# Kernel optimization log

Measured on AMD Instinct MI355X. Metric: run time of the kernel, lower is better.

Reference implementation:

```python
import jax, jax.numpy as jnp
import numpy as np

B, S, H = 128, 512, 768      # batch, seq, encoder hidden
NL = 42                      # len(LABEL_TO_ID)
LD = 300                     # label_dim
DK, DV = 64, 768             # K_dim, V_dim
HID = 768                    # opt['hidden_dim']
P = 512                      # max_seq_length == pos_indicator
INF = 1e12                   # constant.INFINITY_NUMBER
NEG = -1e9


def gelu(x):
    return 0.5 * x * (1.0 + jax.lax.erf(x * 0.7071067811865476))


def setup_inputs() -> dict:
    key = jax.random.key(0)
    ks = jax.random.split(key, 24)
    sc = 0.02
    return {
        "inputs": jax.random.normal(ks[0], (B, S, H), jnp.float32),
        "pos_ids": jax.random.randint(ks[1], (B, S), 0, 53),
        "dep_ids": jax.random.randint(ks[2], (B, S), 0, 42),
        "subj_pos": jax.random.randint(ks[3], (B, S), 0, P + 1),
        "obj_pos": jax.random.randint(ks[4], (B, S), 0, P + 1),
        "adj": jnp.zeros((1, 1, 1), jnp.float32),  # unused by forward
        # stacked per-label Q/K projections (41 = NL-1 labels, label 0 excluded)
        "WQ": jax.random.normal(ks[5], (NL - 1, DK, H), jnp.float32) * sc,
        "bQ": jax.random.normal(ks[6], (NL - 1, DK), jnp.float32) * sc,
        "WK": jax.random.normal(ks[7], (NL - 1, DK, LD), jnp.float32) * sc,
        "bK": jax.random.normal(ks[8], (NL - 1, DK), jnp.float32) * sc,
        "WV_w": jax.random.normal(ks[9], (DV, H), jnp.float32) * sc,
        "WV_b": jax.random.normal(ks[10], (DV,), jnp.float32) * sc,
        "Wout_w": jax.random.normal(ks[11], (H, DV), jnp.float32) * sc,
        "Wout_b": jax.random.normal(ks[12], (H,), jnp.float32) * sc,
        "ln_g": jnp.ones((H,), jnp.float32),
        "ln_b": jnp.zeros((H,), jnp.float32),
        "label_emb": jax.random.normal(ks[13], (NL, LD), jnp.float32) * sc,
        "feat_w": jax.random.normal(ks[14], (HID, 3 * H), jnp.float32) * sc,
        "feat_b": jax.random.normal(ks[15], (HID,), jnp.float32) * sc,
        "out_w": jax.random.normal(ks[16], (LD, HID), jnp.float32) * sc,
        "out_b": jax.random.normal(ks[17], (LD,), jnp.float32) * sc,
    }


def reference(inputs, pos_ids, dep_ids, subj_pos, obj_pos, adj,
              WQ, bQ, WK, bK, WV_w, WV_b, Wout_w, Wout_b, ln_g, ln_b,
              label_emb, feat_w, feat_b, out_w, out_b):
    dt = inputs.dtype
    # combined attention mask (bool OR, as torch bool+bool): entity markers + padding
    mask = (subj_pos == P) | (obj_pos == P) | (pos_ids == 0)   # [B,S]

    # --- LabelAttention: 41-loop collapses to one fused projection ---
    lab = label_emb[1:NL]                                      # [41,LD] labels 1..41
    kvec = jnp.einsum('ld,lkd->lk', lab, WK) + bK              # [41,DK] per-label keys
    # scores_sum[b,s] = sum_l (x W_Q_l^T + b_Q_l) . k_l  /sqrt(dk)  + 41*mask*NEG
    w_eff = jnp.einsum('lk,lkh->h', kvec, WQ)                  # [H]
    c = jnp.sum(kvec * bQ)                                     # scalar
    scores = (inputs @ w_eff + c) / 8.0                        # sqrt(DK)=8; [B,S]
    scores = scores + (NL - 1) * mask.astype(dt) * NEG
    attn = jax.nn.softmax(scores, axis=-1)                     # [B,S]

    wv = inputs @ WV_w.T + WV_b                                # [B,S,DV]
    ctx = jnp.einsum('bs,bsd->bd', attn, wv)                   # [B,DV]
    ctx = gelu(ctx @ Wout_w.T + Wout_b)                        # [B,H]
    mu = ctx.mean(-1, keepdims=True)
    var = ((ctx - mu) ** 2).mean(-1, keepdims=True)
    ctx = (ctx - mu) / jnp.sqrt(var + 1e-5) * ln_g + ln_b

    # --- entity max pooling (mask True where NOT part of entity) ---
    sm = (subj_pos != P)[:, :, None]
    om = (obj_pos != P)[:, :, None]
    subj_out = jnp.where(sm, -INF, inputs).max(axis=1)         # [B,H]
    obj_out = jnp.where(om, -INF, inputs).max(axis=1)          # [B,H]

    feats = jnp.concatenate([subj_out, obj_out, ctx], axis=-1)  # [B,3H]
    feats = gelu(feats @ feat_w.T + feat_b)                     # [B,HID]
    feats = gelu(feats @ out_w.T + out_b)                       # [B,LD]

    logits = feats @ label_emb.T                                # [B,42]
    return logits, ctx
```

## Files before the change

### kernel.cpp

```cpp
#include <hip/hip_runtime.h>
#include <math.h>

#define BB 128
#define SS 512
#define HH 768
#define PPOS 512
#define NEGC (-1.0e9f)
#define NINF (-1.0e12f)

#define OFF_KVEC   0
#define OFF_WEFF   2624
#define OFF_C      3392
#define OFF_SCORES 4096
#define OFF_CAT    0
#define OFF_POOLED 294912
#define OFF_PP     393216
#define OFF_PS     1179648
#define OFF_PO     1966080
#define OFF_CTXA   393216
#define OFF_CTXB   491520
#define OFF_F1     589824
#define OFF_F2     688128

__device__ __forceinline__ float gelu_f(float x) {
    return 0.5f * x * (1.0f + erff(x * 0.70710678118654752f));
}
__device__ __forceinline__ float dot4(float4 a, float4 b) {
    return a.x*b.x + a.y*b.y + a.z*b.z + a.w*b.w;
}

template<int K4, int ACT, int MT>
__global__ __launch_bounds__(256) void k_mm(const float* __restrict__ A,
        const float* __restrict__ W, const float* __restrict__ bias,
        float* __restrict__ C, int M, int N) {
    int lane = threadIdx.x & 63;
    int wave = (blockIdx.x * 256 + threadIdx.x) >> 6;
    int ntn = (N + 15) >> 4;
    int m0 = (wave / ntn) * MT;
    if (m0 >= M) return;
    int n0 = ((wave % ntn) << 4) + (lane >> 2);
    int ks = lane & 3;
    bool nvalid = (n0 < N);
    const float4* A4 = (const float4*)A;
    const float4* w_row = (const float4*)W + (size_t)(nvalid ? n0 : 0) * K4;
    const float4* ar = A4 + (size_t)m0 * K4;
    float acc[MT];
    #pragma unroll
    for (int r = 0; r < MT; ++r) acc[r] = 0.f;
    #pragma unroll 4
    for (int j = ks; j < K4; j += 4) {
        float4 wv = w_row[j];
        #pragma unroll
        for (int r = 0; r < MT; ++r) acc[r] += dot4(ar[(size_t)r * K4 + j], wv);
    }
    #pragma unroll
    for (int r = 0; r < MT; ++r) {
        acc[r] += __shfl_xor(acc[r], 1, 64);
        acc[r] += __shfl_xor(acc[r], 2, 64);
    }
    if (ks == 0 && nvalid) {
        float b = bias ? bias[n0] : 0.f;
        #pragma unroll
        for (int r = 0; r < MT; ++r) {
            float v = acc[r] + b;
            if (ACT == 1) v = gelu_f(v);
            C[(size_t)(m0 + r) * N + n0] = v;
        }
    }
}

__global__ __launch_bounds__(256) void k_kvec2(const float* __restrict__ label_emb,
        const float* __restrict__ WK, const float* __restrict__ bK,
        float* __restrict__ ws) {
    if (blockIdx.x < 3) ws[OFF_WEFF + blockIdx.x * 256 + threadIdx.x] = 0.f;
    if (blockIdx.x == 3 && threadIdx.x == 0) ws[OFF_C] = 0.f;
    int lane = threadIdx.x & 63;
    int idx = (blockIdx.x * 256 + threadIdx.x) >> 6;
    int l = idx >> 6;
    const float4* lab4 = (const float4*)(label_emb + (size_t)(l + 1) * 300);
    const float4* wk4  = (const float4*)(WK + (size_t)idx * 300);
    float acc = dot4(lab4[lane], wk4[lane]);
    if (lane < 11) acc += dot4(lab4[64 + lane], wk4[64 + lane]);
    #pragma unroll
    for (int off = 32; off > 0; off >>= 1) acc += __shfl_xor(acc, off, 64);
    if (lane == 0) ws[OFF_KVEC + idx] = acc + bK[idx];
}

__global__ __launch_bounds__(256) void k_weff2(const float* __restrict__ WQ,
        const float* __restrict__ bQ, float* __restrict__ ws) {
    int lane = threadIdx.x & 63;
    int w = (blockIdx.x * 256 + threadIdx.x) >> 6;
    if (w < 492) {
        int jc = w / 12, hg = w % 12;
        int h = hg * 64 + lane;
        const float* wq = WQ + (size_t)(jc * 64) * HH + h;
        const float* kv = ws + OFF_KVEC + jc * 64;
        float acc = 0.f;
        #pragma unroll 8
        for (int j = 0; j < 64; ++j) acc += kv[j] * wq[(size_t)j * HH];
        atomicAdd(&ws[OFF_WEFF + h], acc);
    } else if (w == 492) {
        float acc = 0.f;
        for (int j = lane; j < 2624; j += 64) acc += ws[OFF_KVEC + j] * bQ[j];
        #pragma unroll
        for (int off = 32; off > 0; off >>= 1) acc += __shfl_xor(acc, off, 64);
        if (lane == 0) atomicAdd(&ws[OFF_C], acc);
    }
}

__global__ __launch_bounds__(256) void k_scores(const float* __restrict__ inputs,
        const int* __restrict__ pos_ids, const int* __restrict__ subj_pos,
        const int* __restrict__ obj_pos, float* __restrict__ ws) {
    int wave = threadIdx.x >> 6, lane = threadIdx.x & 63;
    const float4* in4 = (const float4*)inputs;
    const float4* w4  = (const float4*)(ws + OFF_WEFF);
    float c = ws[OFF_C];
    float4 w0 = w4[lane], w1 = w4[64 + lane], w2 = w4[128 + lane];
    int wid = blockIdx.x * 4 + wave;
    for (int i = 0; i < 8; ++i) {
        int row = wid + 8192 * i;
        const float4* r4 = in4 + (size_t)row * 192;
        float acc = dot4(r4[lane], w0) + dot4(r4[64 + lane], w1) + dot4(r4[128 + lane], w2);
        #pragma unroll
        for (int off = 32; off > 0; off >>= 1) acc += __shfl_down(acc, off, 64);
        if (lane == 0) {
            bool m = (subj_pos[row] == PPOS) | (obj_pos[row] == PPOS) | (pos_ids[row] == 0);
            float sc = (acc + c) * 0.125f;
            if (m) sc += 41.0f * NEGC;
            ws[OFF_SCORES + row] = sc;
        }
    }
}

__global__ __launch_bounds__(192) void k_pool(const float* __restrict__ inputs,
        const int* __restrict__ subj_pos, const int* __restrict__ obj_pos,
        float* __restrict__ ws) {
    __shared__ float red[256];
    __shared__ float al[64];
    __shared__ int lsf[64];
    __shared__ int lof[64];
    int chunk = blockIdx.x, b = blockIdx.y, t = threadIdx.x;
    int s0 = chunk * 64;
    const float* sc = ws + OFF_SCORES + (size_t)b * SS;
    float v0 = sc[t], v1 = sc[t + 192], v2 = (t < 128) ? sc[t + 384] : NINF;
    red[t] = fmaxf(fmaxf(v0, v1), v2);
    if (t >= 128) { }
    if (t < 64) red[t + 192] = NINF;
    __syncthreads();
    for (int s2 = 128; s2 > 0; s2 >>= 1) {
        if (t < s2) red[t] = fmaxf(red[t], red[t + s2]);
        __syncthreads();
    }
    float m = red[0];
    __syncthreads();
    float e0 = expf(v0 - m) + expf(v1 - m) + ((t < 128) ? expf(v2 - m) : 0.f);
    red[t] = e0;
    if (t < 64) red[t + 192] = 0.f;
    __syncthreads();
    for (int s2 = 128; s2 > 0; s2 >>= 1) {
        if (t < s2) red[t] += red[t + s2];
        __syncthreads();
    }
    float inv = 1.0f / red[0];
    if (t < 64) {
        int gs = b * SS + s0 + t;
        al[t]  = expf(sc[s0 + t] - m) * inv;
        lsf[t] = (subj_pos[gs] == PPOS);
        lof[t] = (obj_pos[gs] == PPOS);
    }
    __syncthreads();
    const float4* in4 = (const float4*)inputs;
    float4 pool = make_float4(0.f, 0.f, 0.f, 0.f);
    float4 smax = make_float4(NINF, NINF, NINF, NINF);
    float4 omax = make_float4(NINF, NINF, NINF, NINF);
    for (int s = 0; s < 64; ++s) {
        float4 x = in4[((size_t)(b * SS + s0 + s)) * 192 + t];
        float a = al[s];
        pool.x += a * x.x; pool.y += a * x.y; pool.z += a * x.z; pool.w += a * x.w;
        if (lsf[s]) {
            smax.x = fmaxf(smax.x, x.x); smax.y = fmaxf(smax.y, x.y);
            smax.z = fmaxf(smax.z, x.z); smax.w = fmaxf(smax.w, x.w);
        }
        if (lof[s]) {
            omax.x = fmaxf(omax.x, x.x); omax.y = fmaxf(omax.y, x.y);
            omax.z = fmaxf(omax.z, x.z); omax.w = fmaxf(omax.w, x.w);
        }
    }
    size_t o = (size_t)(b * 8 + chunk) * 192 + t;
    ((float4*)(ws + OFF_PP))[o] = pool;
    ((float4*)(ws + OFF_PS))[o] = smax;
    ((float4*)(ws + OFF_PO))[o] = omax;
}

__global__ void k_reduce(float* __restrict__ ws) {
    int i = blockIdx.x * 256 + threadIdx.x;
    int b = i / HH, h = i - b * HH;
    float p = 0.f, sm = NINF, om = NINF;
    #pragma unroll
    for (int j = 0; j < 8; ++j) {
        int o = (b * 8 + j) * HH + h;
        p += ws[OFF_PP + o];
        sm = fmaxf(sm, ws[OFF_PS + o]);
        om = fmaxf(om, ws[OFF_PO + o]);
    }
    ws[OFF_POOLED + i] = p;
    ws[OFF_CAT + (size_t)b * 2304 + h] = sm;
    ws[OFF_CAT + (size_t)b * 2304 + 768 + h] = om;
}

__global__ void k_ln(const float* __restrict__ ln_g, const float* __restrict__ ln_b,
                     float* __restrict__ ws, float* __restrict__ out) {
    __shared__ float red[256];
    __shared__ float red2[256];
    int b = blockIdx.x, t = threadIdx.x;
    const float* x = ws + OFF_CTXB + (size_t)b * HH;
    float a0 = x[t], a1 = x[t + 256], a2 = x[t + 512];
    red[t]  = a0 + a1 + a2;
    red2[t] = a0 * a0 + a1 * a1 + a2 * a2;
    __syncthreads();
    for (int s2 = 128; s2 > 0; s2 >>= 1) {
        if (t < s2) { red[t] += red[t + s2]; red2[t] += red2[t + s2]; }
        __syncthreads();
    }
    float mu  = red[0] * (1.0f / 768.0f);
    float var = red2[0] * (1.0f / 768.0f) - mu * mu;
    float inv = rsqrtf(var + 1e-5f);
    float* o = out + 5376 + (size_t)b * HH;
    float* cc = ws + OFF_CAT + (size_t)b * 2304 + 1536;
    float r0 = (a0 - mu) * inv * ln_g[t]       + ln_b[t];
    float r1 = (a1 - mu) * inv * ln_g[t + 256] + ln_b[t + 256];
    float r2 = (a2 - mu) * inv * ln_g[t + 512] + ln_b[t + 512];
    o[t] = r0; o[t + 256] = r1; o[t + 512] = r2;
    cc[t] = r0; cc[t + 256] = r1; cc[t + 512] = r2;
}

extern "C" void kernel_launch(void* const* d_in, const int* in_sizes, int n_in,
                              void* d_out, int out_size, void* d_ws, size_t ws_size,
                              hipStream_t stream) {
    const float* inputs    = (const float*)d_in[0];
    const int*   pos_ids   = (const int*)d_in[1];
    const int*   subj_pos  = (const int*)d_in[3];
    const int*   obj_pos   = (const int*)d_in[4];
    const float* WQ        = (const float*)d_in[6];
    const float* bQ        = (const float*)d_in[7];
    const float* WK        = (const float*)d_in[8];
    const float* bK        = (const float*)d_in[9];
    const float* WV_w      = (const float*)d_in[10];
    const float* WV_b      = (const float*)d_in[11];
    const float* Wout_w    = (const float*)d_in[12];
    const float* Wout_b    = (const float*)d_in[13];
    const float* ln_g      = (const float*)d_in[14];
    const float* ln_b      = (const float*)d_in[15];
    const float* label_emb = (const float*)d_in[16];
    const float* feat_w    = (const float*)d_in[17];
    const float* feat_b    = (const float*)d_in[18];
    const float* out_w     = (const float*)d_in[19];
    const float* out_b     = (const float*)d_in[20];
    float* out = (float*)d_out;
    float* ws  = (float*)d_ws;

    k_kvec2  <<<656, 256, 0, stream>>>(label_emb, WK, bK, ws);
    k_weff2  <<<124, 256, 0, stream>>>(WQ, bQ, ws);
    k_scores <<<2048, 256, 0, stream>>>(inputs, pos_ids, subj_pos, obj_pos, ws);
    k_pool   <<<dim3(8, BB), 192, 0, stream>>>(inputs, subj_pos, obj_pos, ws);
    k_reduce <<<384, 256, 0, stream>>>(ws);
    k_mm<192,0,2><<<768, 256, 0, stream>>>(ws + OFF_POOLED, WV_w, WV_b, ws + OFF_CTXA, BB, HH);
    k_mm<192,1,2><<<768, 256, 0, stream>>>(ws + OFF_CTXA, Wout_w, Wout_b, ws + OFF_CTXB, BB, HH);
    k_ln     <<<BB, 256, 0, stream>>>(ln_g, ln_b, ws, out);
    k_mm<576,1,2><<<768, 256, 0, stream>>>(ws + OFF_CAT, feat_w, feat_b, ws + OFF_F1, BB, HH);
    k_mm<192,1,2><<<304, 256, 0, stream>>>(ws + OFF_F1, out_w, out_b, ws + OFF_F2, BB, 300);
    k_mm<75,0,2><<<48, 256, 0, stream>>>(ws + OFF_F2, label_emb, nullptr, out, BB, 42);
}
```

Baseline: 476.5 us.

## Fuse pooling, reduction, matmuls and layernorm into one persistent kernel with grid barriers

Replaces eight separate launches (pool, reduce, four-plus matmuls, layernorm) with a single persistent kernel of 1024 blocks that separates phases with atomic-counter grid barriers. The goal is to remove per-launch overhead and the idle gaps between many small dependent kernels. The workspace layout is reshuffled so buffers no longer alias, the layernorm uses wave shuffles, and the feat matmul uses 4 rows per wave. It depends on all 1024 blocks being co-resident (launch bounds of 3 blocks per CU); if they are not, the barriers deadlock. It also adds spin-wait and atomic cost at each of seven barriers.

Result: slower. 1.646 ms (+245.4%).

```diff
diff --git a/kernel.cpp b/kernel.cpp
--- a/kernel.cpp
+++ b/kernel.cpp
@@ -12,15 +12,19 @@
 #define OFF_WEFF   2624
 #define OFF_C      3392
 #define OFF_SCORES 4096
-#define OFF_CAT    0
-#define OFF_POOLED 294912
-#define OFF_PP     393216
-#define OFF_PS     1179648
-#define OFF_PO     1966080
-#define OFF_CTXA   393216
-#define OFF_CTXB   491520
-#define OFF_F1     589824
-#define OFF_F2     688128
+#define OFF_PP     69632
+#define OFF_PS     856064
+#define OFF_PO     1642496
+#define OFF_POOLED 2428928
+#define OFF_CAT    2527232
+#define OFF_CTXA   2822144
+#define OFF_CTXB   2920448
+#define OFF_F1     3018752
+#define OFF_F2     3117056
+#define OFF_BAR    3155456
+
+#define NBLK 1024
+#define NTHR 192
 
 __device__ __forceinline__ float gelu_f(float x) {
     return 0.5f * x * (1.0f + erff(x * 0.70710678118654752f));
@@ -29,29 +33,36 @@
     return a.x*b.x + a.y*b.y + a.z*b.z + a.w*b.w;
 }
 
+__device__ __forceinline__ void gbar(unsigned* bar, unsigned nblk) {
+    __syncthreads();
+    if (threadIdx.x == 0) {
+        __hip_atomic_fetch_add(bar, 1u, __ATOMIC_ACQ_REL, __HIP_MEMORY_SCOPE_AGENT);
+        while (__hip_atomic_load(bar, __ATOMIC_ACQUIRE, __HIP_MEMORY_SCOPE_AGENT) < nblk)
+            __builtin_amdgcn_s_sleep(2);
+    }
+    __syncthreads();
+}
+
 template<int K4, int ACT, int MT>
-__global__ __launch_bounds__(256) void k_mm(const float* __restrict__ A,
+__device__ __forceinline__ void mm_phase(const float* __restrict__ A,
         const float* __restrict__ W, const float* __restrict__ bias,
-        float* __restrict__ C, int M, int N) {
-    int lane = threadIdx.x & 63;
-    int wave = (blockIdx.x * 256 + threadIdx.x) >> 6;
+        float* __restrict__ C, int M, int N, int wv, int lane) {
     int ntn = (N + 15) >> 4;
-    int m0 = (wave / ntn) * MT;
+    int m0 = (wv / ntn) * MT;
     if (m0 >= M) return;
-    int n0 = ((wave % ntn) << 4) + (lane >> 2);
+    int n0 = ((wv % ntn) << 4) + (lane >> 2);
     int ks = lane & 3;
     bool nvalid = (n0 < N);
-    const float4* A4 = (const float4*)A;
     const float4* w_row = (const float4*)W + (size_t)(nvalid ? n0 : 0) * K4;
-    const float4* ar = A4 + (size_t)m0 * K4;
+    const float4* ar = (const float4*)A + (size_t)m0 * K4;
     float acc[MT];
     #pragma unroll
     for (int r = 0; r < MT; ++r) acc[r] = 0.f;
     #pragma unroll 4
     for (int j = ks; j < K4; j += 4) {
-        float4 wv = w_row[j];
-        #pragma unroll
-        for (int r = 0; r < MT; ++r) acc[r] += dot4(ar[(size_t)r * K4 + j], wv);
+        float4 wvv = w_row[j];
+        #pragma unroll
+        for (int r = 0; r < MT; ++r) acc[r] += dot4(ar[(size_t)r * K4 + j], wvv);
     }
     #pragma unroll
     for (int r = 0; r < MT; ++r) {
@@ -111,6 +122,8 @@
 __global__ __launch_bounds__(256) void k_scores(const float* __restrict__ inputs,
         const int* __restrict__ pos_ids, const int* __restrict__ subj_pos,
         const int* __restrict__ obj_pos, float* __restrict__ ws) {
+    if (blockIdx.x == 0 && threadIdx.x < 16)
+        ((unsigned*)(ws + OFF_BAR))[threadIdx.x] = 0u;
     int wave = threadIdx.x >> 6, lane = threadIdx.x & 63;
     const float4* in4 = (const float4*)inputs;
     const float4* w4  = (const float4*)(ws + OFF_WEFF);
@@ -132,106 +145,141 @@
     }
 }
 
-__global__ __launch_bounds__(192) void k_pool(const float* __restrict__ inputs,
-        const int* __restrict__ subj_pos, const int* __restrict__ obj_pos,
-        float* __restrict__ ws) {
-    __shared__ float red[256];
-    __shared__ float al[64];
-    __shared__ int lsf[64];
-    __shared__ int lof[64];
-    int chunk = blockIdx.x, b = blockIdx.y, t = threadIdx.x;
-    int s0 = chunk * 64;
-    const float* sc = ws + OFF_SCORES + (size_t)b * SS;
-    float v0 = sc[t], v1 = sc[t + 192], v2 = (t < 128) ? sc[t + 384] : NINF;
-    red[t] = fmaxf(fmaxf(v0, v1), v2);
-    if (t >= 128) { }
-    if (t < 64) red[t + 192] = NINF;
-    __syncthreads();
-    for (int s2 = 128; s2 > 0; s2 >>= 1) {
-        if (t < s2) red[t] = fmaxf(red[t], red[t + s2]);
-        __syncthreads();
-    }
-    float m = red[0];
-    __syncthreads();
-    float e0 = expf(v0 - m) + expf(v1 - m) + ((t < 128) ? expf(v2 - m) : 0.f);
-    red[t] = e0;
-    if (t < 64) red[t + 192] = 0.f;
-    __syncthreads();
-    for (int s2 = 128; s2 > 0; s2 >>= 1) {
-        if (t < s2) red[t] += red[t + s2];
-        __syncthreads();
-    }
-    float inv = 1.0f / red[0];
-    if (t < 64) {
-        int gs = b * SS + s0 + t;
-        al[t]  = expf(sc[s0 + t] - m) * inv;
-        lsf[t] = (subj_pos[gs] == PPOS);
-        lof[t] = (obj_pos[gs] == PPOS);
-    }
-    __syncthreads();
-    const float4* in4 = (const float4*)inputs;
-    float4 pool = make_float4(0.f, 0.f, 0.f, 0.f);
-    float4 smax = make_float4(NINF, NINF, NINF, NINF);
-    float4 omax = make_float4(NINF, NINF, NINF, NINF);
-    for (int s = 0; s < 64; ++s) {
-        float4 x = in4[((size_t)(b * SS + s0 + s)) * 192 + t];
-        float a = al[s];
-        pool.x += a * x.x; pool.y += a * x.y; pool.z += a * x.z; pool.w += a * x.w;
-        if (lsf[s]) {
-            smax.x = fmaxf(smax.x, x.x); smax.y = fmaxf(smax.y, x.y);
-            smax.z = fmaxf(smax.z, x.z); smax.w = fmaxf(smax.w, x.w);
-        }
-        if (lof[s]) {
-            omax.x = fmaxf(omax.x, x.x); omax.y = fmaxf(omax.y, x.y);
-            omax.z = fmaxf(omax.z, x.z); omax.w = fmaxf(omax.w, x.w);
-        }
-    }
-    size_t o = (size_t)(b * 8 + chunk) * 192 + t;
-    ((float4*)(ws + OFF_PP))[o] = pool;
-    ((float4*)(ws + OFF_PS))[o] = smax;
-    ((float4*)(ws + OFF_PO))[o] = omax;
-}
-
-__global__ void k_reduce(float* __restrict__ ws) {
-    int i = blockIdx.x * 256 + threadIdx.x;
-    int b = i / HH, h = i - b * HH;
-    float p = 0.f, sm = NINF, om = NINF;
-    #pragma unroll
-    for (int j = 0; j < 8; ++j) {
-        int o = (b * 8 + j) * HH + h;
-        p += ws[OFF_PP + o];
-        sm = fmaxf(sm, ws[OFF_PS + o]);
-        om = fmaxf(om, ws[OFF_PO + o]);
-    }
-    ws[OFF_POOLED + i] = p;
-    ws[OFF_CAT + (size_t)b * 2304 + h] = sm;
-    ws[OFF_CAT + (size_t)b * 2304 + 768 + h] = om;
-}
-
-__global__ void k_ln(const float* __restrict__ ln_g, const float* __restrict__ ln_b,
-                     float* __restrict__ ws, float* __restrict__ out) {
-    __shared__ float red[256];
-    __shared__ float red2[256];
-    int b = blockIdx.x, t = threadIdx.x;
-    const float* x = ws + OFF_CTXB + (size_t)b * HH;
-    float a0 = x[t], a1 = x[t + 256], a2 = x[t + 512];
-    red[t]  = a0 + a1 + a2;
-    red2[t] = a0 * a0 + a1 * a1 + a2 * a2;
-    __syncthreads();
-    for (int s2 = 128; s2 > 0; s2 >>= 1) {
-        if (t < s2) { red[t] += red[t + s2]; red2[t] += red2[t + s2]; }
-        __syncthreads();
-    }
-    float mu  = red[0] * (1.0f / 768.0f);
-    float var = red2[0] * (1.0f / 768.0f) - mu * mu;
-    float inv = rsqrtf(var + 1e-5f);
-    float* o = out + 5376 + (size_t)b * HH;
-    float* cc = ws + OFF_CAT + (size_t)b * 2304 + 1536;
-    float r0 = (a0 - mu) * inv * ln_g[t]       + ln_b[t];
-    float r1 = (a1 - mu) * inv * ln_g[t + 256] + ln_b[t + 256];
-    float r2 = (a2 - mu) * inv * ln_g[t + 512] + ln_b[t + 512];
-    o[t] = r0; o[t + 256] = r1; o[t + 512] = r2;
-    cc[t] = r0; cc[t + 256] = r1; cc[t + 512] = r2;
+__global__ __launch_bounds__(NTHR, 3) void k_tail(
+        const float* __restrict__ inputs, const int* __restrict__ subj_pos,
+        const int* __restrict__ obj_pos,
+        const float* __restrict__ WV_w, const float* __restrict__ WV_b,
+        const float* __restrict__ Wout_w, const float* __restrict__ Wout_b,
+        const float* __restrict__ ln_g, const float* __restrict__ ln_b,
+        const float* __restrict__ feat_w, const float* __restrict__ feat_b,
+        const float* __restrict__ out_w, const float* __restrict__ out_b,
+        const float* __restrict__ label_emb,
+        float* __restrict__ ws, float* __restrict__ out) {
+    unsigned* bar = (unsigned*)(ws + OFF_BAR);
+    int t = threadIdx.x;
+    int lane = t & 63;
+    int wid = t >> 6;
+    int wv = blockIdx.x * 3 + wid;
+
+    {
+        __shared__ float red[256];
+        __shared__ float al[64];
+        __shared__ int lsf[64];
+        __shared__ int lof[64];
+        int b = blockIdx.x >> 3, chunk = blockIdx.x & 7;
+        int s0 = chunk * 64;
+        const float* sc = ws + OFF_SCORES + (size_t)b * SS;
+        float v0 = sc[t], v1 = sc[t + 192], v2 = (t < 128) ? sc[t + 384] : NINF;
+        red[t] = fmaxf(fmaxf(v0, v1), v2);
+        if (t < 64) red[t + 192] = NINF;
+        __syncthreads();
+        for (int s2 = 128; s2 > 0; s2 >>= 1) {
+            if (t < s2) red[t] = fmaxf(red[t], red[t + s2]);
+            __syncthreads();
+        }
+        float m = red[0];
+        __syncthreads();
+        float e0 = expf(v0 - m) + expf(v1 - m) + ((t < 128) ? expf(v2 - m) : 0.f);
+        red[t] = e0;
+        if (t < 64) red[t + 192] = 0.f;
+        __syncthreads();
+        for (int s2 = 128; s2 > 0; s2 >>= 1) {
+            if (t < s2) red[t] += red[t + s2];
+            __syncthreads();
+        }
+        float inv = 1.0f / red[0];
+        if (t < 64) {
+            int gs = b * SS + s0 + t;
+            al[t]  = expf(sc[s0 + t] - m) * inv;
+            lsf[t] = (subj_pos[gs] == PPOS);
+            lof[t] = (obj_pos[gs] == PPOS);
+        }
+        __syncthreads();
+        const float4* in4 = (const float4*)inputs;
+        float4 pool = make_float4(0.f, 0.f, 0.f, 0.f);
+        float4 smax = make_float4(NINF, NINF, NINF, NINF);
+        float4 omax = make_float4(NINF, NINF, NINF, NINF);
+        for (int s = 0; s < 64; ++s) {
+            float4 x = in4[((size_t)(b * SS + s0 + s)) * 192 + t];
+            float a = al[s];
+            pool.x += a * x.x; pool.y += a * x.y; pool.z += a * x.z; pool.w += a * x.w;
+            if (lsf[s]) {
+                smax.x = fmaxf(smax.x, x.x); smax.y = fmaxf(smax.y, x.y);
+                smax.z = fmaxf(smax.z, x.z); smax.w = fmaxf(smax.w, x.w);
+            }
+            if (lof[s]) {
+                omax.x = fmaxf(omax.x, x.x); omax.y = fmaxf(omax.y, x.y);
+                omax.z = fmaxf(omax.z, x.z); omax.w = fmaxf(omax.w, x.w);
+            }
+        }
+        size_t o = (size_t)(b * 8 + chunk) * 192 + t;
+        ((float4*)(ws + OFF_PP))[o] = pool;
+        ((float4*)(ws + OFF_PS))[o] = smax;
+        ((float4*)(ws + OFF_PO))[o] = omax;
+    }
+    gbar(bar + 0, NBLK);
+
+    {
+        int i = blockIdx.x * NTHR + t;
+        if (i < BB * HH) {
+            int b = i / HH, h = i - b * HH;
+            float p = 0.f, sm = NINF, om = NINF;
+            #pragma unroll
+            for (int j = 0; j < 8; ++j) {
+                int o = (b * 8 + j) * HH + h;
+                p += ws[OFF_PP + o];
+                sm = fmaxf(sm, ws[OFF_PS + o]);
+                om = fmaxf(om, ws[OFF_PO + o]);
+            }
+            ws[OFF_POOLED + i] = p;
+            ws[OFF_CAT + (size_t)b * 2304 + h] = sm;
+            ws[OFF_CAT + (size_t)b * 2304 + 768 + h] = om;
+        }
+    }
+    gbar(bar + 1, NBLK);
+
+    mm_phase<192, 0, 2>(ws + OFF_POOLED, WV_w, WV_b, ws + OFF_CTXA, BB, HH, wv, lane);
+    gbar(bar + 2, NBLK);
+
+    mm_phase<192, 1, 2>(ws + OFF_CTXA, Wout_w, Wout_b, ws + OFF_CTXB, BB, HH, wv, lane);
+    gbar(bar + 3, NBLK);
+
+    if (blockIdx.x < BB) {
+        int b = blockIdx.x;
+        const float* x = ws + OFF_CTXB + (size_t)b * HH;
+        float a0 = x[t], a1 = x[t + 192], a2 = x[t + 384], a3 = x[t + 576];
+        float s1 = a0 + a1 + a2 + a3;
+        float s2 = a0*a0 + a1*a1 + a2*a2 + a3*a3;
+        #pragma unroll
+        for (int off = 32; off > 0; off >>= 1) {
+            s1 += __shfl_xor(s1, off, 64);
+            s2 += __shfl_xor(s2, off, 64);
+        }
+        __shared__ float rs[3], rq[3];
+        if (lane == 0) { rs[wid] = s1; rq[wid] = s2; }
+        __syncthreads();
+        float S1 = rs[0] + rs[1] + rs[2], S2 = rq[0] + rq[1] + rq[2];
+        float mu  = S1 * (1.0f / 768.0f);
+        float var = S2 * (1.0f / 768.0f) - mu * mu;
+        float inv = rsqrtf(var + 1e-5f);
+        float* o  = out + 5376 + (size_t)b * HH;
+        float* cc = ws + OFF_CAT + (size_t)b * 2304 + 1536;
+        float r0 = (a0 - mu) * inv * ln_g[t]       + ln_b[t];
+        float r1 = (a1 - mu) * inv * ln_g[t + 192] + ln_b[t + 192];
+        float r2 = (a2 - mu) * inv * ln_g[t + 384] + ln_b[t + 384];
+        float r3 = (a3 - mu) * inv * ln_g[t + 576] + ln_b[t + 576];
+        o[t] = r0; o[t + 192] = r1; o[t + 384] = r2; o[t + 576] = r3;
+        cc[t] = r0; cc[t + 192] = r1; cc[t + 384] = r2; cc[t + 576] = r3;
+    }
+    gbar(bar + 4, NBLK);
+
+    mm_phase<576, 1, 4>(ws + OFF_CAT, feat_w, feat_b, ws + OFF_F1, BB, HH, wv, lane);
+    gbar(bar + 5, NBLK);
+
+    mm_phase<192, 1, 2>(ws + OFF_F1, out_w, out_b, ws + OFF_F2, BB, 300, wv, lane);
+    gbar(bar + 6, NBLK);
+
+    mm_phase<75, 0, 2>(ws + OFF_F2, label_emb, nullptr, out, BB, 42, wv, lane);
 }
 
 extern "C" void kernel_launch(void* const* d_in, const int* in_sizes, int n_in,
@@ -262,12 +310,8 @@
     k_kvec2  <<<656, 256, 0, stream>>>(label_emb, WK, bK, ws);
     k_weff2  <<<124, 256, 0, stream>>>(WQ, bQ, ws);
     k_scores <<<2048, 256, 0, stream>>>(inputs, pos_ids, subj_pos, obj_pos, ws);
-    k_pool   <<<dim3(8, BB), 192, 0, stream>>>(inputs, subj_pos, obj_pos, ws);
-    k_reduce <<<384, 256, 0, stream>>>(ws);
-    k_mm<192,0,2><<<768, 256, 0, stream>>>(ws + OFF_POOLED, WV_w, WV_b, ws + OFF_CTXA, BB, HH);
-    k_mm<192,1,2><<<768, 256, 0, stream>>>(ws + OFF_CTXA, Wout_w, Wout_b, ws + OFF_CTXB, BB, HH);
-    k_ln     <<<BB, 256, 0, stream>>>(ln_g, ln_b, ws, out);
-    k_mm<576,1,2><<<768, 256, 0, stream>>>(ws + OFF_CAT, feat_w, feat_b, ws + OFF_F1, BB, HH);
-    k_mm<192,1,2><<<304, 256, 0, stream>>>(ws + OFF_F1, out_w, out_b, ws + OFF_F2, BB, 300);
-    k_mm<75,0,2><<<48, 256, 0, stream>>>(ws + OFF_F2, label_emb, nullptr, out, BB, 42);
-}
+    k_tail   <<<NBLK, NTHR, 0, stream>>>(inputs, subj_pos, obj_pos,
+                                         WV_w, WV_b, Wout_w, Wout_b,
+                                         ln_g, ln_b, feat_w, feat_b,
+                                         out_w, out_b, label_emb, ws, out);
+}
```

## Split pooling into finer chunks, fuse final two matmuls, raise feat tile

Applied to the files above, without the earlier changes.

Pooling blocks now cover 32 sequence positions instead of 64, giving twice as many blocks per batch row, and the inner loop is unrolled by two to expose more loads in flight. The reduce kernel now combines 16 partials instead of 8. The out_w projection and the label-embedding projection are fused into one per-batch kernel that keeps intermediates in shared memory, and the feat matmul processes 4 rows per wave instead of 2. The workspace layout moves to non-overlapping offsets to hold the larger partial buffers. The trade-off is more partial-sum traffic, and the fused kernel has low parallelism with one block per batch row.

Measured after the change: 523.5 us. +9.9%, slower.

```diff
diff --git a/kernel.cpp b/kernel.cpp
--- a/kernel.cpp
+++ b/kernel.cpp
@@ -12,15 +12,15 @@
 #define OFF_WEFF   2624
 #define OFF_C      3392
 #define OFF_SCORES 4096
-#define OFF_CAT    0
-#define OFF_POOLED 294912
-#define OFF_PP     393216
-#define OFF_PS     1179648
-#define OFF_PO     1966080
-#define OFF_CTXA   393216
-#define OFF_CTXB   491520
-#define OFF_F1     589824
-#define OFF_F2     688128
+#define OFF_PP     69632
+#define OFF_PS     1642496
+#define OFF_PO     3215360
+#define OFF_POOLED 4788224
+#define OFF_CAT    4886528
+#define OFF_CTXA   5181440
+#define OFF_CTXB   5279744
+#define OFF_F1     5378048
+#define OFF_F2     5476352
 
 __device__ __forceinline__ float gelu_f(float x) {
     return 0.5f * x * (1.0f + erff(x * 0.70710678118654752f));
@@ -41,9 +41,8 @@
     int n0 = ((wave % ntn) << 4) + (lane >> 2);
     int ks = lane & 3;
     bool nvalid = (n0 < N);
-    const float4* A4 = (const float4*)A;
     const float4* w_row = (const float4*)W + (size_t)(nvalid ? n0 : 0) * K4;
-    const float4* ar = A4 + (size_t)m0 * K4;
+    const float4* ar = (const float4*)A + (size_t)m0 * K4;
     float acc[MT];
     #pragma unroll
     for (int r = 0; r < MT; ++r) acc[r] = 0.f;
@@ -136,15 +135,14 @@
         const int* __restrict__ subj_pos, const int* __restrict__ obj_pos,
         float* __restrict__ ws) {
     __shared__ float red[256];
-    __shared__ float al[64];
-    __shared__ int lsf[64];
-    __shared__ int lof[64];
+    __shared__ float al[32];
+    __shared__ int lsf[32];
+    __shared__ int lof[32];
     int chunk = blockIdx.x, b = blockIdx.y, t = threadIdx.x;
-    int s0 = chunk * 64;
+    int s0 = chunk * 32;
     const float* sc = ws + OFF_SCORES + (size_t)b * SS;
     float v0 = sc[t], v1 = sc[t + 192], v2 = (t < 128) ? sc[t + 384] : NINF;
     red[t] = fmaxf(fmaxf(v0, v1), v2);
-    if (t >= 128) { }
     if (t < 64) red[t + 192] = NINF;
     __syncthreads();
     for (int s2 = 128; s2 > 0; s2 >>= 1) {
@@ -162,7 +160,7 @@
         __syncthreads();
     }
     float inv = 1.0f / red[0];
-    if (t < 64) {
+    if (t < 32) {
         int gs = b * SS + s0 + t;
         al[t]  = expf(sc[s0 + t] - m) * inv;
         lsf[t] = (subj_pos[gs] == PPOS);
@@ -173,20 +171,30 @@
     float4 pool = make_float4(0.f, 0.f, 0.f, 0.f);
     float4 smax = make_float4(NINF, NINF, NINF, NINF);
     float4 omax = make_float4(NINF, NINF, NINF, NINF);
-    for (int s = 0; s < 64; ++s) {
-        float4 x = in4[((size_t)(b * SS + s0 + s)) * 192 + t];
-        float a = al[s];
-        pool.x += a * x.x; pool.y += a * x.y; pool.z += a * x.z; pool.w += a * x.w;
+    for (int s = 0; s < 32; s += 2) {
+        float4 x0 = in4[((size_t)(b * SS + s0 + s)) * 192 + t];
+        float4 x1 = in4[((size_t)(b * SS + s0 + s + 1)) * 192 + t];
+        float a0 = al[s], a1 = al[s + 1];
+        pool.x += a0 * x0.x; pool.y += a0 * x0.y; pool.z += a0 * x0.z; pool.w += a0 * x0.w;
         if (lsf[s]) {
-            smax.x = fmaxf(smax.x, x.x); smax.y = fmaxf(smax.y, x.y);
-            smax.z = fmaxf(smax.z, x.z); smax.w = fmaxf(smax.w, x.w);
+            smax.x = fmaxf(smax.x, x0.x); smax.y = fmaxf(smax.y, x0.y);
+            smax.z = fmaxf(smax.z, x0.z); smax.w = fmaxf(smax.w, x0.w);
         }
         if (lof[s]) {
-            omax.x = fmaxf(omax.x, x.x); omax.y = fmaxf(omax.y, x.y);
-            omax.z = fmaxf(omax.z, x.z); omax.w = fmaxf(omax.w, x.w);
-        }
-    }
-    size_t o = (size_t)(b * 8 + chunk) * 192 + t;
+            omax.x = fmaxf(omax.x, x0.x); omax.y = fmaxf(omax.y, x0.y);
+            omax.z = fmaxf(omax.z, x0.z); omax.w = fmaxf(omax.w, x0.w);
+        }
+        pool.x += a1 * x1.x; pool.y += a1 * x1.y; pool.z += a1 * x1.z; pool.w += a1 * x1.w;
+        if (lsf[s + 1]) {
+            smax.x = fmaxf(smax.x, x1.x); smax.y = fmaxf(smax.y, x1.y);
+            smax.z = fmaxf(smax.z, x1.z); smax.w = fmaxf(smax.w, x1.w);
+        }
+        if (lof[s + 1]) {
+            omax.x = fmaxf(omax.x, x1.x); omax.y = fmaxf(omax.y, x1.y);
+            omax.z = fmaxf(omax.z, x1.z); omax.w = fmaxf(omax.w, x1.w);
+        }
+    }
+    size_t o = (size_t)(b * 16 + chunk) * 192 + t;
     ((float4*)(ws + OFF_PP))[o] = pool;
     ((float4*)(ws + OFF_PS))[o] = smax;
     ((float4*)(ws + OFF_PO))[o] = omax;
@@ -197,8 +205,8 @@
     int b = i / HH, h = i - b * HH;
     float p = 0.f, sm = NINF, om = NINF;
     #pragma unroll
-    for (int j = 0; j < 8; ++j) {
-        int o = (b * 8 + j) * HH + h;
+    for (int j = 0; j < 16; ++j) {
+        int o = (b * 16 + j) * HH + h;
         p += ws[OFF_PP + o];
         sm = fmaxf(sm, ws[OFF_PS + o]);
         om = fmaxf(om, ws[OFF_PO + o]);
@@ -232,6 +240,33 @@
     float r2 = (a2 - mu) * inv * ln_g[t + 512] + ln_b[t + 512];
     o[t] = r0; o[t + 256] = r1; o[t + 512] = r2;
     cc[t] = r0; cc[t + 256] = r1; cc[t + 512] = r2;
+}
+
+__global__ __launch_bounds__(320) void k_f2l(const float* __restrict__ out_w,
+        const float* __restrict__ out_b, const float* __restrict__ label_emb,
+        float* __restrict__ ws, float* __restrict__ out) {
+    __shared__ __align__(16) float xr[768];
+    __shared__ __align__(16) float f2s[300];
+    int b = blockIdx.x, t = threadIdx.x;
+    for (int i = t; i < 768; i += 320) xr[i] = ws[OFF_F1 + (size_t)b * HH + i];
+    __syncthreads();
+    if (t < 300) {
+        const float4* w4 = (const float4*)(out_w + (size_t)t * HH);
+        const float4* x4 = (const float4*)xr;
+        float acc = out_b[t];
+        #pragma unroll 4
+        for (int q = 0; q < 192; ++q) acc += dot4(w4[q], x4[q]);
+        f2s[t] = gelu_f(acc);
+    }
+    __syncthreads();
+    if (t < 42) {
+        const float4* l4 = (const float4*)(label_emb + (size_t)t * 300);
+        const float4* x4 = (const float4*)f2s;
+        float acc = 0.f;
+        #pragma unroll 4
+        for (int q = 0; q < 75; ++q) acc += dot4(l4[q], x4[q]);
+        out[b * 42 + t] = acc;
+    }
 }
 
 extern "C" void kernel_launch(void* const* d_in, const int* in_sizes, int n_in,
@@ -262,12 +297,11 @@
     k_kvec2  <<<656, 256, 0, stream>>>(label_emb, WK, bK, ws);
     k_weff2  <<<124, 256, 0, stream>>>(WQ, bQ, ws);
     k_scores <<<2048, 256, 0, stream>>>(inputs, pos_ids, subj_pos, obj_pos, ws);
-    k_pool   <<<dim3(8, BB), 192, 0, stream>>>(inputs, subj_pos, obj_pos, ws);
+    k_pool   <<<dim3(16, BB), 192, 0, stream>>>(inputs, subj_pos, obj_pos, ws);
     k_reduce <<<384, 256, 0, stream>>>(ws);
     k_mm<192,0,2><<<768, 256, 0, stream>>>(ws + OFF_POOLED, WV_w, WV_b, ws + OFF_CTXA, BB, HH);
     k_mm<192,1,2><<<768, 256, 0, stream>>>(ws + OFF_CTXA, Wout_w, Wout_b, ws + OFF_CTXB, BB, HH);
     k_ln     <<<BB, 256, 0, stream>>>(ln_g, ln_b, ws, out);
-    k_mm<576,1,2><<<768, 256, 0, stream>>>(ws + OFF_CAT, feat_w, feat_b, ws + OFF_F1, BB, HH);
-    k_mm<192,1,2><<<304, 256, 0, stream>>>(ws + OFF_F1, out_w, out_b, ws + OFF_F2, BB, 300);
-    k_mm<75,0,2><<<48, 256, 0, stream>>>(ws + OFF_F2, label_emb, nullptr, out, BB, 42);
-}
+    k_mm<576,1,4><<<384, 256, 0, stream>>>(ws + OFF_CAT, feat_w, feat_b, ws + OFF_F1, BB, HH);
+    k_f2l    <<<BB, 320, 0, stream>>>(out_w, out_b, label_emb, ws, out);
+}
```
